# Kernel optimization log

Measured on AMD Instinct MI355X. Metric: run time of the kernel, lower is better.

Reference implementation:

```python
import jax, jax.numpy as jnp
import numpy as np

NIN = 1024
NOUT = 1024
NHEADS = 16
DHEAD = NOUT // NHEADS


def setup_inputs() -> dict:
    key = jax.random.key(0)
    k1, k2, k3, k4 = jax.random.split(key, 4)
    y = jax.random.normal(k1, (2, 2048, NIN), dtype=jnp.float32)
    Wqkv = jax.random.normal(k2, (NIN, 3 * NOUT), dtype=jnp.float32) * (1.0 / np.sqrt(NIN))
    Wff = jax.random.normal(k3, (NOUT, NOUT), dtype=jnp.float32) * (1.0 / np.sqrt(NOUT))
    bff = jax.random.normal(k4, (NOUT,), dtype=jnp.float32) * 0.01
    return {"y": y, "Wqkv": Wqkv, "Wff": Wff, "bff": bff}


def reference(y, Wqkv, Wff, bff):
    b, n, _ = y.shape
    qkv = y @ Wqkv  # [b, n, 3*nout]
    qkv = qkv.reshape(b, n, 3, NHEADS, DHEAD).transpose(2, 0, 3, 1, 4)
    q, k, v = qkv[0], qkv[1], qkv[2]  # each [b, h, n, d]
    att = jnp.einsum('bhqd,bhkd->bhqk', q, k)
    causal = jnp.triu(jnp.ones((n, n), dtype=bool), k=1)
    att = jnp.where(causal, -jnp.inf, att)
    att = jax.nn.softmax(att / jnp.sqrt(jnp.float32(DHEAD)), axis=-1)
    ctx = jnp.einsum('bhqk,bhkd->bhqd', att, v)
    ctx = ctx.transpose(0, 2, 1, 3).reshape(b, n, NOUT)
    return ctx @ Wff + bff
```

## Files before the change

kernel.cpp:

```cpp
#include <hip/hip_runtime.h>
#include <stdint.h>

#define NHEADS 16
#define DHEAD 64
#define SEQ 2048
#define BATCH 2
#define NINF 1024
#define NOUTF 1024
#define N3 3072
#define MTOT 4096

typedef unsigned short US;
typedef __attribute__((ext_vector_type(8))) short short8;
typedef __attribute__((ext_vector_type(4))) short short4v;
typedef __attribute__((ext_vector_type(4))) float f32x4;

#if __has_builtin(__builtin_amdgcn_exp2f)
#define EXP2(x) __builtin_amdgcn_exp2f(x)
#else
#define EXP2(x) exp2f(x)
#endif

__device__ inline US f2bf(float f) {
  union { float f; unsigned u; } v; v.f = f;
  unsigned r = v.u + 0x7fffu + ((v.u >> 16) & 1u);
  return (US)(r >> 16);
}

__device__ inline f32x4 mfma16(short8 a, short8 b, f32x4 c) {
  return __builtin_amdgcn_mfma_f32_16x16x32_bf16(a, b, c, 0, 0, 0);
}

__device__ inline f32x4 mfma16k16(short4v a, short4v b, f32x4 c) {
  return __builtin_amdgcn_mfma_f32_16x16x16bf16_1k(a, b, c, 0, 0, 0);
}

__device__ inline void async16(const US* g, US* l) {
  __builtin_amdgcn_global_load_lds(
      (const __attribute__((address_space(1))) unsigned int*)g,
      (__attribute__((address_space(3))) unsigned int*)l, 16, 0, 0);
}

__global__ void k_convert(const float* __restrict__ src, US* __restrict__ dst, int n4) {
  int i = blockIdx.x * blockDim.x + threadIdx.x;
  if (i >= n4) return;
  float4 v = ((const float4*)src)[i];
  ushort4 o;
  o.x = f2bf(v.x); o.y = f2bf(v.y); o.z = f2bf(v.z); o.w = f2bf(v.w);
  ((ushort4*)dst)[i] = o;
}

__global__ void k_wtrans(const float* __restrict__ Wqkv, const float* __restrict__ Wff,
                         US* __restrict__ dq, US* __restrict__ df) {
  __shared__ float tile[32][33];
  int bxi = blockIdx.x;
  const float* src; US* dst; int C;
  if (bxi < 96) { src = Wqkv; dst = dq; C = N3; }
  else          { src = Wff;  dst = df; C = NOUTF; bxi -= 96; }
  int bx = bxi * 32, by = blockIdx.y * 32;
  int tx = threadIdx.x, ty = threadIdx.y;
  for (int i = 0; i < 32; i += 8)
    tile[ty + i][tx] = src[(size_t)(by + ty + i) * C + bx + tx];
  __syncthreads();
  for (int i = 0; i < 32; i += 8)
    dst[(size_t)(bx + ty + i) * 1024 + by + tx] = f2bf(tile[tx][ty + i]);
}

__global__ void k_vtrans(const US* __restrict__ src, US* __restrict__ dst) {
  __shared__ US tile[32][33];
  int bh = blockIdx.z;
  int bx = blockIdx.x * 32;
  int by = blockIdx.y * 32;
  int tx = threadIdx.x, ty = threadIdx.y;
  const US* s0 = src + (size_t)bh * SEQ * DHEAD;
  US* d0 = dst + (size_t)bh * DHEAD * SEQ;
  for (int i = 0; i < 32; i += 8)
    tile[ty + i][tx] = s0[(size_t)(by + ty + i) * DHEAD + bx + tx];
  __syncthreads();
  for (int i = 0; i < 32; i += 8)
    d0[(size_t)(bx + ty + i) * SEQ + by + tx] = tile[tx][ty + i];
}

__global__ __launch_bounds__(256) void k_gemm_qkv(
    const US* __restrict__ A,
    const US* __restrict__ Bt,
    US* __restrict__ qbuf, US* __restrict__ kbuf, US* __restrict__ vbuf) {
  __shared__ US As[128 * 32];
  __shared__ US Bs[128 * 32];
  int tid = threadIdx.x;
  int wave = tid >> 6, lane = tid & 63, lm = lane & 15, lk = lane >> 4;
  int wm = wave >> 1, wn = wave & 1;
  int mbase = blockIdx.y * 128, nbase = blockIdx.x * 128;

  f32x4 acc[4][4];
#pragma unroll
  for (int i = 0; i < 4; ++i)
#pragma unroll
    for (int j = 0; j < 4; ++j) acc[i][j] = (f32x4){0.f, 0.f, 0.f, 0.f};

  const US* ga = A + (size_t)(mbase + (tid >> 2)) * NINF + (tid & 3) * 8;
  const US* gb = Bt + (size_t)(nbase + (tid >> 2)) * NINF + (tid & 3) * 8;
  US* la = As + tid * 8;
  US* lb = Bs + tid * 8;

  for (int kt = 0; kt < NINF / 32; ++kt) {
    int ko = kt * 32;
    async16(ga + ko, la);
    async16(ga + ko + (size_t)64 * NINF, la + 64 * 32);
    async16(gb + ko, lb);
    async16(gb + ko + (size_t)64 * NINF, lb + 64 * 32);
    __syncthreads();
    short8 a[4], b[4];
#pragma unroll
    for (int i = 0; i < 4; ++i)
      a[i] = *(const short8*)(As + (wm * 64 + i * 16 + lm) * 32 + lk * 8);
#pragma unroll
    for (int j = 0; j < 4; ++j)
      b[j] = *(const short8*)(Bs + (wn * 64 + j * 16 + lm) * 32 + lk * 8);
#pragma unroll
    for (int i = 0; i < 4; ++i)
#pragma unroll
      for (int j = 0; j < 4; ++j) acc[i][j] = mfma16(a[i], b[j], acc[i][j]);
    __syncthreads();
  }

  int which = nbase >> 10;
  US* dsts = (which == 0) ? qbuf : (which == 1) ? kbuf : vbuf;
  float sc = (which == 0) ? 0.18033688011112042f : 1.f;
#pragma unroll
  for (int j = 0; j < 4; ++j) {
    int col = nbase + wn * 64 + j * 16 + lm;
    int hh = (col & 1023) >> 6;
    int d = col & 63;
#pragma unroll
    for (int i = 0; i < 4; ++i) {
#pragma unroll
      for (int r = 0; r < 4; ++r) {
        int row = mbase + wm * 64 + i * 16 + lk * 4 + r;
        int bb = row >> 11;
        int s = row & (SEQ - 1);
        int bh = bb * NHEADS + hh;
        dsts[((size_t)bh * SEQ + s) * DHEAD + d] = f2bf(acc[i][j][r] * sc);
      }
    }
  }
}

__global__ __launch_bounds__(128, 2) void k_attn(
    const US* __restrict__ qbuf, const US* __restrict__ kbuf,
    const US* __restrict__ vtbuf, US* __restrict__ ctx) {
  __shared__ US Ks[64 * 64];
  __shared__ US Vs[64 * 64];
  int tid = threadIdx.x;
  int w = tid >> 6, lane = tid & 63;
  int lm = lane & 15, lk = lane >> 4;
  int bl = blockIdx.x;
  int xcd = bl & 7, g2 = bl >> 3;
  int bh = (g2 & 3) * 8 + xcd;
  int s = 31 - (g2 >> 2);
  int qb = s * 64 + w * 32;
  int nt = s + 1;

  const US* kbase = kbuf + (size_t)bh * SEQ * DHEAD;
  const US* vtb = vtbuf + (size_t)bh * DHEAD * SEQ;
  const US* q_base = qbuf + (size_t)bh * SEQ * DHEAD;

  short8 qf[2][2];
#pragma unroll
  for (int g = 0; g < 2; ++g) {
    const US* qr = q_base + (size_t)(qb + g * 16 + lm) * DHEAD + lk * 8;
    qf[g][0] = *(const short8*)(qr);
    qf[g][1] = *(const short8*)(qr + 32);
  }

  int swz = ((lane & 7) ^ (lane >> 3)) * 8;
  const US* gK[4]; const US* gV[4];
  US* dKl[4]; US* dVl[4];
#pragma unroll
  for (int j = 0; j < 4; ++j) {
    int u = w * 4 + j;
    gK[j] = kbase + (size_t)(u * 8 + (lane >> 3)) * DHEAD + swz;
    dKl[j] = Ks + u * 512 + lane * 8;
    gV[j] = vtb + (size_t)(u * 8 + (lane >> 3)) * SEQ + swz;
    dVl[j] = Vs + u * 512 + lane * 8;
  }

  int xorv = lm & 7;
  int ck0 = ((lk) ^ xorv) * 16;
  int ck1 = ((4 + lk) ^ xorv) * 16;
  const short4v kones = {(short)0x3F80, (short)0x3F80, (short)0x3F80, (short)0x3F80};

  f32x4 o[2][4];
#pragma unroll
  for (int g = 0; g < 2; ++g)
#pragma unroll
    for (int dg = 0; dg < 4; ++dg) o[g][dg] = (f32x4){0.f, 0.f, 0.f, 0.f};
  f32x4 lacc[2];
  lacc[0] = (f32x4){0.f, 0.f, 0.f, 0.f};
  lacc[1] = (f32x4){0.f, 0.f, 0.f, 0.f};

  const char* Kc = (const char*)Ks;
  const char* Vc = (const char*)Vs;

  auto body = [&](int kg, bool act0, bool dm0, bool dm1) {
    const char* kr = Kc + (kg * 16 + lm) * 128;
    short8 ka0 = *(const short8*)(kr + ck0);
    short8 ka1 = *(const short8*)(kr + ck1);
    short4v pk[2];
    bool act[2] = {act0, true};
    bool dm[2] = {dm0, dm1};
#pragma unroll
    for (int g = 0; g < 2; ++g) {
      if (!act[g]) continue;
      f32x4 st = (f32x4){0.f, 0.f, 0.f, 0.f};
      st = mfma16(ka0, qf[g][0], st);
      st = mfma16(ka1, qf[g][1], st);
      uint32_t ue[4];
#pragma unroll
      for (int r = 0; r < 4; ++r) {
        float v = st[r];
        if (dm[g] && (lk * 4 + r > lm)) v = -INFINITY;
        union { float f; uint32_t u; } cv2;
        cv2.f = EXP2(v);
        ue[r] = cv2.u + 0x8000u;
      }
      union { short4v s4; uint32_t u[2]; } pz;
      pz.u[0] = __builtin_amdgcn_perm(ue[1], ue[0], 0x07060302u);
      pz.u[1] = __builtin_amdgcn_perm(ue[3], ue[2], 0x07060302u);
      pk[g] = pz.s4;
      lacc[g] = mfma16k16(kones, pk[g], lacc[g]);
    }
    int cvo = (((kg * 2 + (lk >> 1)) ^ xorv) * 16) + (lk & 1) * 8;
    const char* vr = Vc + lm * 128 + cvo;
#pragma unroll
    for (int dg = 0; dg < 4; ++dg) {
      short4v va = *(const short4v*)(vr + dg * 2048);
      if (act0) o[0][dg] = mfma16k16(va, pk[0], o[0][dg]);
      o[1][dg] = mfma16k16(va, pk[1], o[1][dg]);
    }
  };

  for (int t = 0; t < nt; ++t) {
    __syncthreads();
#pragma unroll
    for (int j = 0; j < 4; ++j) { async16(gK[j], dKl[j]); async16(gV[j], dVl[j]); }
#pragma unroll
    for (int j = 0; j < 4; ++j) { gK[j] += 64 * DHEAD; gV[j] += 64; }
    __syncthreads();

    if (t < nt - 1) {
#pragma unroll
      for (int kg = 0; kg < 4; ++kg) body(kg, true, false, false);
    } else {
      int kmax = 2 * w + 1;
      for (int kg = 0; kg <= kmax; ++kg)
        body(kg, kg <= 2 * w, kg == 2 * w, kg == kmax);
    }
  }

  US* cb = ctx + (size_t)(bh >> 4) * SEQ * NOUTF + (bh & 15) * DHEAD;
#pragma unroll
  for (int g = 0; g < 2; ++g) {
    float inv = 1.f / lacc[g][0];
    US* crow = cb + (size_t)(qb + g * 16 + lm) * NOUTF;
#pragma unroll
    for (int dg = 0; dg < 4; ++dg) {
      union { short4v s4; uint32_t u[2]; } pz;
      pz.u[0] = (uint32_t)f2bf(o[g][dg][0] * inv) | ((uint32_t)f2bf(o[g][dg][1] * inv) << 16);
      pz.u[1] = (uint32_t)f2bf(o[g][dg][2] * inv) | ((uint32_t)f2bf(o[g][dg][3] * inv) << 16);
      *(short4v*)(crow + dg * 16 + lk * 4) = pz.s4;
    }
  }
}

__global__ __launch_bounds__(256) void k_gemm_out(
    const US* __restrict__ A, const US* __restrict__ Bt,
    const float* __restrict__ bias, float* __restrict__ out) {
  __shared__ US As[128 * 32];
  __shared__ US Bs[64 * 32];
  int tid = threadIdx.x;
  int wave = tid >> 6, lane = tid & 63, lm = lane & 15, lk = lane >> 4;
  int mbase = blockIdx.y * 128, nbase = blockIdx.x * 64;

  f32x4 acc[2][4];
#pragma unroll
  for (int i = 0; i < 2; ++i)
#pragma unroll
    for (int j = 0; j < 4; ++j) acc[i][j] = (f32x4){0.f, 0.f, 0.f, 0.f};

  const US* ga = A + (size_t)(mbase + (tid >> 2)) * NOUTF + (tid & 3) * 8;
  const US* gb = Bt + (size_t)(nbase + (tid >> 2)) * NOUTF + (tid & 3) * 8;
  US* la = As + tid * 8;
  US* lb = Bs + tid * 8;

  for (int kt = 0; kt < NOUTF / 32; ++kt) {
    int ko = kt * 32;
    async16(ga + ko, la);
    async16(ga + ko + (size_t)64 * NOUTF, la + 64 * 32);
    async16(gb + ko, lb);
    __syncthreads();
    short8 a[2], b[4];
#pragma unroll
    for (int i = 0; i < 2; ++i)
      a[i] = *(const short8*)(As + (wave * 32 + i * 16 + lm) * 32 + lk * 8);
#pragma unroll
    for (int j = 0; j < 4; ++j)
      b[j] = *(const short8*)(Bs + (j * 16 + lm) * 32 + lk * 8);
#pragma unroll
    for (int i = 0; i < 2; ++i)
#pragma unroll
      for (int j = 0; j < 4; ++j) acc[i][j] = mfma16(a[i], b[j], acc[i][j]);
    __syncthreads();
  }

#pragma unroll
  for (int j = 0; j < 4; ++j) {
    int col = nbase + j * 16 + lm;
    float bv = bias[col];
#pragma unroll
    for (int i = 0; i < 2; ++i)
#pragma unroll
      for (int r = 0; r < 4; ++r) {
        int row = mbase + wave * 32 + i * 16 + lk * 4 + r;
        out[(size_t)row * NOUTF + col] = acc[i][j][r] + bv;
      }
  }
}

extern "C" void kernel_launch(void* const* d_in, const int* in_sizes, int n_in,
                              void* d_out, int out_size, void* d_ws, size_t ws_size,
                              hipStream_t stream) {
  const float* y    = (const float*)d_in[0];
  const float* Wqkv = (const float*)d_in[1];
  const float* Wff  = (const float*)d_in[2];
  const float* bff  = (const float*)d_in[3];
  float* out = (float*)d_out;

  char* ws = (char*)d_ws;
  US* ybf   = (US*)(ws);
  US* ctx   = (US*)(ws);
  US* wqkvt = (US*)(ws + (8u << 20));
  US* wfft  = (US*)(ws + (14u << 20));
  US* qbuf  = (US*)(ws + (16u << 20));
  US* kbuf  = (US*)(ws + (24u << 20));
  US* vbuf  = (US*)(ws + (32u << 20));
  US* vtbuf = (US*)(ws + (40u << 20));

  k_convert<<<MTOT * NINF / 4 / 256, 256, 0, stream>>>(y, ybf, MTOT * NINF / 4);
  k_wtrans<<<dim3(128, 32), dim3(32, 8), 0, stream>>>(Wqkv, Wff, wqkvt, wfft);
  k_gemm_qkv<<<dim3(N3 / 128, MTOT / 128), 256, 0, stream>>>(ybf, wqkvt, qbuf, kbuf, vbuf);
  k_vtrans<<<dim3(DHEAD / 32, SEQ / 32, BATCH * NHEADS), dim3(32, 8), 0, stream>>>(vbuf, vtbuf);
  k_attn<<<dim3(1024), 128, 0, stream>>>(qbuf, kbuf, vtbuf, ctx);
  k_gemm_out<<<dim3(NOUTF / 64, MTOT / 128), 256, 0, stream>>>(ctx, wfft, bff, out);
}
```

Baseline: 194.1 us.

## Fuse V transpose into QKV GEMM epilogue and double-buffer attention K/V tiles

The QKV GEMM now writes V directly in transposed [bh, d, seq] layout, which removes the separate k_vtrans kernel and its extra global round trip. For Q/K tiles it swaps the MFMA operand order so each lane holds four consecutive d values and can store them as packed 8-byte vectors instead of scalar 2-byte stores. The attention kernel double-buffers K/V tiles in LDS, prefetching the next tile asynchronously while computing the current one. This doubles the LDS footprint per block, which may affect occupancy.

```diff
diff --git a/kernel.cpp b/kernel.cpp
--- a/kernel.cpp
+++ b/kernel.cpp
@@ -25,6 +25,10 @@
   union { float f; unsigned u; } v; v.f = f;
   unsigned r = v.u + 0x7fffu + ((v.u >> 16) & 1u);
   return (US)(r >> 16);
+}
+
+__device__ inline uint32_t pack2(float a, float b) {
+  return (uint32_t)f2bf(a) | ((uint32_t)f2bf(b) << 16);
 }
 
 __device__ inline f32x4 mfma16(short8 a, short8 b, f32x4 c) {
@@ -66,31 +70,17 @@
     dst[(size_t)(bx + ty + i) * 1024 + by + tx] = f2bf(tile[tx][ty + i]);
 }
 
-__global__ void k_vtrans(const US* __restrict__ src, US* __restrict__ dst) {
-  __shared__ US tile[32][33];
-  int bh = blockIdx.z;
-  int bx = blockIdx.x * 32;
-  int by = blockIdx.y * 32;
-  int tx = threadIdx.x, ty = threadIdx.y;
-  const US* s0 = src + (size_t)bh * SEQ * DHEAD;
-  US* d0 = dst + (size_t)bh * DHEAD * SEQ;
-  for (int i = 0; i < 32; i += 8)
-    tile[ty + i][tx] = s0[(size_t)(by + ty + i) * DHEAD + bx + tx];
-  __syncthreads();
-  for (int i = 0; i < 32; i += 8)
-    d0[(size_t)(bx + ty + i) * SEQ + by + tx] = tile[tx][ty + i];
-}
-
 __global__ __launch_bounds__(256) void k_gemm_qkv(
     const US* __restrict__ A,
     const US* __restrict__ Bt,
-    US* __restrict__ qbuf, US* __restrict__ kbuf, US* __restrict__ vbuf) {
+    US* __restrict__ qbuf, US* __restrict__ kbuf, US* __restrict__ vtbuf) {
   __shared__ US As[128 * 32];
   __shared__ US Bs[128 * 32];
   int tid = threadIdx.x;
   int wave = tid >> 6, lane = tid & 63, lm = lane & 15, lk = lane >> 4;
   int wm = wave >> 1, wn = wave & 1;
   int mbase = blockIdx.y * 128, nbase = blockIdx.x * 128;
+  bool vout = (nbase >= 2048);
 
   f32x4 acc[4][4];
 #pragma unroll
@@ -117,30 +107,51 @@
 #pragma unroll
     for (int j = 0; j < 4; ++j)
       b[j] = *(const short8*)(Bs + (wn * 64 + j * 16 + lm) * 32 + lk * 8);
-#pragma unroll
-    for (int i = 0; i < 4; ++i)
-#pragma unroll
-      for (int j = 0; j < 4; ++j) acc[i][j] = mfma16(a[i], b[j], acc[i][j]);
+    if (vout) {
+#pragma unroll
+      for (int i = 0; i < 4; ++i)
+#pragma unroll
+        for (int j = 0; j < 4; ++j) acc[i][j] = mfma16(a[i], b[j], acc[i][j]);
+    } else {
+#pragma unroll
+      for (int i = 0; i < 4; ++i)
+#pragma unroll
+        for (int j = 0; j < 4; ++j) acc[i][j] = mfma16(b[j], a[i], acc[i][j]);
+    }
     __syncthreads();
   }
 
   int which = nbase >> 10;
-  US* dsts = (which == 0) ? qbuf : (which == 1) ? kbuf : vbuf;
-  float sc = (which == 0) ? 0.18033688011112042f : 1.f;
-#pragma unroll
-  for (int j = 0; j < 4; ++j) {
-    int col = nbase + wn * 64 + j * 16 + lm;
-    int hh = (col & 1023) >> 6;
-    int d = col & 63;
+  int hh = ((nbase + wn * 64) & 1023) >> 6;
+  if (!vout) {
+    US* dsts = (which == 0) ? qbuf : kbuf;
+    float sc = (which == 0) ? 0.18033688011112042f : 1.f;
 #pragma unroll
     for (int i = 0; i < 4; ++i) {
-#pragma unroll
-      for (int r = 0; r < 4; ++r) {
-        int row = mbase + wm * 64 + i * 16 + lk * 4 + r;
-        int bb = row >> 11;
-        int s = row & (SEQ - 1);
-        int bh = bb * NHEADS + hh;
-        dsts[((size_t)bh * SEQ + s) * DHEAD + d] = f2bf(acc[i][j][r] * sc);
+      int row = mbase + wm * 64 + i * 16 + lm;
+      int bb = row >> 11, s = row & (SEQ - 1);
+      US* rb = dsts + ((size_t)(bb * NHEADS + hh) * SEQ + s) * DHEAD;
+#pragma unroll
+      for (int j = 0; j < 4; ++j) {
+        int dbase = j * 16 + lk * 4;
+        union { short4v s4; uint32_t u[2]; } pz;
+        pz.u[0] = pack2(acc[i][j][0] * sc, acc[i][j][1] * sc);
+        pz.u[1] = pack2(acc[i][j][2] * sc, acc[i][j][3] * sc);
+        *(short4v*)(rb + dbase) = pz.s4;
+      }
+    }
+  } else {
+#pragma unroll
+    for (int j = 0; j < 4; ++j) {
+      int d = j * 16 + lm;
+#pragma unroll
+      for (int i = 0; i < 4; ++i) {
+        int r0 = mbase + wm * 64 + i * 16 + lk * 4;
+        int bb = r0 >> 11, s0 = r0 & (SEQ - 1);
+        union { short4v s4; uint32_t u[2]; } pz;
+        pz.u[0] = pack2(acc[i][j][0], acc[i][j][1]);
+        pz.u[1] = pack2(acc[i][j][2], acc[i][j][3]);
+        *(short4v*)(vtbuf + ((size_t)(bb * NHEADS + hh) * DHEAD + d) * SEQ + s0) = pz.s4;
       }
     }
   }
@@ -149,8 +160,8 @@
 __global__ __launch_bounds__(128, 2) void k_attn(
     const US* __restrict__ qbuf, const US* __restrict__ kbuf,
     const US* __restrict__ vtbuf, US* __restrict__ ctx) {
-  __shared__ US Ks[64 * 64];
-  __shared__ US Vs[64 * 64];
+  __shared__ US Ks[2][64 * 64];
+  __shared__ US Vs[2][64 * 64];
   int tid = threadIdx.x;
   int w = tid >> 6, lane = tid & 63;
   int lm = lane & 15, lk = lane >> 4;
@@ -180,9 +191,9 @@
   for (int j = 0; j < 4; ++j) {
     int u = w * 4 + j;
     gK[j] = kbase + (size_t)(u * 8 + (lane >> 3)) * DHEAD + swz;
-    dKl[j] = Ks + u * 512 + lane * 8;
+    dKl[j] = Ks[0] + u * 512 + lane * 8;
     gV[j] = vtb + (size_t)(u * 8 + (lane >> 3)) * SEQ + swz;
-    dVl[j] = Vs + u * 512 + lane * 8;
+    dVl[j] = Vs[0] + u * 512 + lane * 8;
   }
 
   int xorv = lm & 7;
@@ -199,54 +210,63 @@
   lacc[0] = (f32x4){0.f, 0.f, 0.f, 0.f};
   lacc[1] = (f32x4){0.f, 0.f, 0.f, 0.f};
 
-  const char* Kc = (const char*)Ks;
-  const char* Vc = (const char*)Vs;
-
-  auto body = [&](int kg, bool act0, bool dm0, bool dm1) {
-    const char* kr = Kc + (kg * 16 + lm) * 128;
-    short8 ka0 = *(const short8*)(kr + ck0);
-    short8 ka1 = *(const short8*)(kr + ck1);
-    short4v pk[2];
-    bool act[2] = {act0, true};
-    bool dm[2] = {dm0, dm1};
-#pragma unroll
-    for (int g = 0; g < 2; ++g) {
-      if (!act[g]) continue;
-      f32x4 st = (f32x4){0.f, 0.f, 0.f, 0.f};
-      st = mfma16(ka0, qf[g][0], st);
-      st = mfma16(ka1, qf[g][1], st);
-      uint32_t ue[4];
-#pragma unroll
-      for (int r = 0; r < 4; ++r) {
-        float v = st[r];
-        if (dm[g] && (lk * 4 + r > lm)) v = -INFINITY;
-        union { float f; uint32_t u; } cv2;
-        cv2.f = EXP2(v);
-        ue[r] = cv2.u + 0x8000u;
-      }
-      union { short4v s4; uint32_t u[2]; } pz;
-      pz.u[0] = __builtin_amdgcn_perm(ue[1], ue[0], 0x07060302u);
-      pz.u[1] = __builtin_amdgcn_perm(ue[3], ue[2], 0x07060302u);
-      pk[g] = pz.s4;
-      lacc[g] = mfma16k16(kones, pk[g], lacc[g]);
-    }
-    int cvo = (((kg * 2 + (lk >> 1)) ^ xorv) * 16) + (lk & 1) * 8;
-    const char* vr = Vc + lm * 128 + cvo;
-#pragma unroll
-    for (int dg = 0; dg < 4; ++dg) {
-      short4v va = *(const short4v*)(vr + dg * 2048);
-      if (act0) o[0][dg] = mfma16k16(va, pk[0], o[0][dg]);
-      o[1][dg] = mfma16k16(va, pk[1], o[1][dg]);
-    }
-  };
+#pragma unroll
+  for (int j = 0; j < 4; ++j) { async16(gK[j], dKl[j]); async16(gV[j], dVl[j]); }
+#pragma unroll
+  for (int j = 0; j < 4; ++j) { gK[j] += 64 * DHEAD; gV[j] += 64; }
+  __syncthreads();
 
   for (int t = 0; t < nt; ++t) {
-    __syncthreads();
-#pragma unroll
-    for (int j = 0; j < 4; ++j) { async16(gK[j], dKl[j]); async16(gV[j], dVl[j]); }
-#pragma unroll
-    for (int j = 0; j < 4; ++j) { gK[j] += 64 * DHEAD; gV[j] += 64; }
-    __syncthreads();
+    int cur = t & 1, nxt = cur ^ 1;
+    if (t + 1 < nt) {
+#pragma unroll
+      for (int j = 0; j < 4; ++j) {
+        async16(gK[j], dKl[j] + nxt * 4096);
+        async16(gV[j], dVl[j] + nxt * 4096);
+      }
+#pragma unroll
+      for (int j = 0; j < 4; ++j) { gK[j] += 64 * DHEAD; gV[j] += 64; }
+    }
+
+    const char* Kc = (const char*)Ks[cur];
+    const char* Vc = (const char*)Vs[cur];
+    auto body = [&](int kg, bool act0, bool dm0, bool dm1) {
+      const char* kr = Kc + (kg * 16 + lm) * 128;
+      short8 ka0 = *(const short8*)(kr + ck0);
+      short8 ka1 = *(const short8*)(kr + ck1);
+      short4v pk[2];
+      bool act[2] = {act0, true};
+      bool dm[2] = {dm0, dm1};
+#pragma unroll
+      for (int g = 0; g < 2; ++g) {
+        if (!act[g]) continue;
+        f32x4 st = (f32x4){0.f, 0.f, 0.f, 0.f};
+        st = mfma16(ka0, qf[g][0], st);
+        st = mfma16(ka1, qf[g][1], st);
+        uint32_t ue[4];
+#pragma unroll
+        for (int r = 0; r < 4; ++r) {
+          float v = st[r];
+          if (dm[g] && (lk * 4 + r > lm)) v = -INFINITY;
+          union { float f; uint32_t u; } cv2;
+          cv2.f = EXP2(v);
+          ue[r] = cv2.u + 0x8000u;
+        }
+        union { short4v s4; uint32_t u[2]; } pz;
+        pz.u[0] = __builtin_amdgcn_perm(ue[1], ue[0], 0x07060302u);
+        pz.u[1] = __builtin_amdgcn_perm(ue[3], ue[2], 0x07060302u);
+        pk[g] = pz.s4;
+        lacc[g] = mfma16k16(kones, pk[g], lacc[g]);
+      }
+      int cvo = (((kg * 2 + (lk >> 1)) ^ xorv) * 16) + (lk & 1) * 8;
+      const char* vr = Vc + lm * 128 + cvo;
+#pragma unroll
+      for (int dg = 0; dg < 4; ++dg) {
+        short4v va = *(const short4v*)(vr + dg * 2048);
+        if (act0) o[0][dg] = mfma16k16(va, pk[0], o[0][dg]);
+        o[1][dg] = mfma16k16(va, pk[1], o[1][dg]);
+      }
+    };
 
     if (t < nt - 1) {
 #pragma unroll
@@ -256,6 +276,7 @@
       for (int kg = 0; kg <= kmax; ++kg)
         body(kg, kg <= 2 * w, kg == 2 * w, kg == kmax);
     }
+    __syncthreads();
   }
 
   US* cb = ctx + (size_t)(bh >> 4) * SEQ * NOUTF + (bh & 15) * DHEAD;
@@ -266,8 +287,8 @@
 #pragma unroll
     for (int dg = 0; dg < 4; ++dg) {
       union { short4v s4; uint32_t u[2]; } pz;
-      pz.u[0] = (uint32_t)f2bf(o[g][dg][0] * inv) | ((uint32_t)f2bf(o[g][dg][1] * inv) << 16);
-      pz.u[1] = (uint32_t)f2bf(o[g][dg][2] * inv) | ((uint32_t)f2bf(o[g][dg][3] * inv) << 16);
+      pz.u[0] = pack2(o[g][dg][0] * inv, o[g][dg][1] * inv);
+      pz.u[1] = pack2(o[g][dg][2] * inv, o[g][dg][3] * inv);
       *(short4v*)(crow + dg * 16 + lk * 4) = pz.s4;
     }
   }
@@ -343,13 +364,11 @@
   US* wfft  = (US*)(ws + (14u << 20));
   US* qbuf  = (US*)(ws + (16u << 20));
   US* kbuf  = (US*)(ws + (24u << 20));
-  US* vbuf  = (US*)(ws + (32u << 20));
-  US* vtbuf = (US*)(ws + (40u << 20));
+  US* vtbuf = (US*)(ws + (32u << 20));
 
   k_convert<<<MTOT * NINF / 4 / 256, 256, 0, stream>>>(y, ybf, MTOT * NINF / 4);
   k_wtrans<<<dim3(128, 32), dim3(32, 8), 0, stream>>>(Wqkv, Wff, wqkvt, wfft);
-  k_gemm_qkv<<<dim3(N3 / 128, MTOT / 128), 256, 0, stream>>>(ybf, wqkvt, qbuf, kbuf, vbuf);
-  k_vtrans<<<dim3(DHEAD / 32, SEQ / 32, BATCH * NHEADS), dim3(32, 8), 0, stream>>>(vbuf, vtbuf);
+  k_gemm_qkv<<<dim3(N3 / 128, MTOT / 128), 256, 0, stream>>>(ybf, wqkvt, qbuf, kbuf, vtbuf);
   k_attn<<<dim3(1024), 128, 0, stream>>>(qbuf, kbuf, vtbuf, ctx);
   k_gemm_out<<<dim3(NOUTF / 64, MTOT / 128), 256, 0, stream>>>(ctx, wfft, bff, out);
 }
```

Result: slower. 200.4 us (+3.2%).
